# Kernel tuning notes

Hardware: AMD Instinct MI355X
Metric: run time of the kernel (lower is better)

The kernel has to match this reference:

```python
import jax, jax.numpy as jnp
import numpy as np

NUM_QUERIES = 256  # num_queries init arg
D = 256            # decoder_dim


def fps(xyz, n):
    """Furthest point sampling, matching the CUDA furthest_point_sample kernel:
    start at index 0, keep running min squared distance, pick argmax each step.
    xyz: [B, N, 3] -> indices [B, n] int32."""
    B, N, _ = xyz.shape

    def step(carry, _):
        dist, far = carry
        centroid = jnp.take_along_axis(xyz, far[:, None, None], axis=1)  # [B,1,3]
        d = jnp.sum((xyz - centroid) ** 2, axis=-1)                      # [B,N]
        dist = jnp.minimum(dist, d)
        return (dist, jnp.argmax(dist, axis=-1).astype(jnp.int32)), far

    init = (jnp.full((B, N), 1e10, xyz.dtype), jnp.zeros((B,), jnp.int32))
    _, inds = jax.lax.scan(step, init, None, length=n)
    return jnp.transpose(inds)  # [B, n]


def setup_inputs() -> dict:
    key = jax.random.key(0)
    ks = jax.random.split(key, 6)
    B, N = 64, 32768
    # scene coords in roughly [-3, 3]^3 meters
    encoder_xyz = jax.random.uniform(ks[0], (B, N, 3), jnp.float32) * 6.0 - 3.0
    pc_min = jnp.min(encoder_xyz, axis=1)  # [B,3]
    pc_max = jnp.max(encoder_xyz, axis=1)  # [B,3]
    gauss_B = jax.random.normal(ks[1], (3, D // 2), jnp.float32)  # fourier freqs
    W1 = jax.random.normal(ks[2], (D, D), jnp.float32) / np.sqrt(D)
    b1 = jnp.zeros((D,), jnp.float32)
    W2 = jax.random.normal(ks[3], (D, D), jnp.float32) / np.sqrt(D)
    b2 = jnp.zeros((D,), jnp.float32)
    return dict(encoder_xyz=encoder_xyz, pc_min=pc_min, pc_max=pc_max,
                gauss_B=gauss_B, W1=W1, b1=b1, W2=W2, b2=b2)


def reference(encoder_xyz, pc_min, pc_max, gauss_B, W1, b1, W2, b2):
    # --- query selection: FPS + gather (indices are non-differentiable) ---
    inds = fps(jax.lax.stop_gradient(encoder_xyz), NUM_QUERIES)          # [B,nq]
    query_xyz = jnp.take_along_axis(encoder_xyz, inds[..., None], axis=1)  # [B,nq,3]
    # --- PositionEmbeddingCoordsSine (fourier, normalize=True) ---
    norm = (query_xyz - pc_min[:, None, :]) / (pc_max - pc_min)[:, None, :]
    proj = (2.0 * jnp.pi) * jnp.einsum('bnd,df->bnf', norm, gauss_B)     # [B,nq,D/2]
    pos = jnp.concatenate([jnp.sin(proj), jnp.cos(proj)], axis=-1)       # [B,nq,D]
    pos = jnp.transpose(pos, (0, 2, 1))                                   # [B,D,nq]
    # --- query_projection GenericMLP: conv1x1 + ReLU, conv1x1 + output ReLU ---
    h = jax.nn.relu(jnp.einsum('bcn,dc->bdn', pos, W1) + b1[:, None])
    query_embed = jax.nn.relu(jnp.einsum('bcn,dc->bdn', h, W2) + b2[:, None])
    return query_xyz, query_embed
```

## Files before the change

kernel.cpp:

```cpp
#include <hip/hip_runtime.h>

#define FPS_N 32768
#define FPS_T 256
#define NBLK 8
#define PPB (FPS_N / NBLK)
#define PPT (PPB / FPS_T)
#define NCH (PPT / 4)
#define NQ 256
#define DD 256
#define NT 64
#define B_BATCH 64

#define WS_CLEAR_BYTES (B_BATCH * NQ * NBLK * 8)

__global__ __attribute__((amdgpu_flat_work_group_size(FPS_T, FPS_T),
                          amdgpu_waves_per_eu(2, 2)))
void fps_kernel(const float* __restrict__ xyz, float* __restrict__ qout,
                unsigned long long* __restrict__ gslot) {
  const int gid = blockIdx.x;
  const int xcd = gid & 7;
  const int s = gid >> 3;
  const int b = xcd + 8 * (s >> 3);
  const int q = s & 7;
  const int t = threadIdx.x;

  const float* __restrict__ base = xyz + (size_t)b * (FPS_N * 3);
  const float4* __restrict__ base4 =
      (const float4*)(base + (size_t)q * PPB * 3) + (size_t)t * (PPT * 3 / 4);
  float* qb = qout + (size_t)b * (NQ * 3);
  unsigned long long* bslot = gslot + (size_t)b * (NQ * NBLK);

  __shared__ unsigned long long sred[FPS_T / 64];
  __shared__ float4 bc;

  float4 C[PPT * 3 / 4];
#pragma unroll
  for (int i = 0; i < PPT * 3 / 4; ++i) C[i] = base4[i];
#pragma unroll
  for (int i = 0; i < PPT * 3 / 4; ++i) {
    asm volatile("" : "+v"(C[i].x), "+v"(C[i].y), "+v"(C[i].z), "+v"(C[i].w));
  }
  float4 Dst[NCH];
#pragma unroll
  for (int c = 0; c < NCH; ++c) Dst[c] = make_float4(1e10f, 1e10f, 1e10f, 1e10f);

  if (q == 0 && t == 0) { qb[0] = base[0]; qb[1] = base[1]; qb[2] = base[2]; }
  float cx = base[0], cy = base[1], cz = base[2];

#pragma unroll 1
  for (int j = 1; j < NQ; ++j) {
    float best = -1.0f;
    int bik = 0;

#pragma unroll
    for (int c = 0; c < NCH; ++c) {
      const float4 a4 = C[3 * c + 0];
      const float4 b4 = C[3 * c + 1];
      const float4 c4 = C[3 * c + 2];
      const float px[4] = {a4.x, a4.w, b4.z, c4.y};
      const float py[4] = {a4.y, b4.x, b4.w, c4.z};
      const float pz[4] = {a4.z, b4.y, c4.x, c4.w};
      const float dold[4] = {Dst[c].x, Dst[c].y, Dst[c].z, Dst[c].w};
      float dnew[4];
#pragma unroll
      for (int i = 0; i < 4; ++i) {
        const float dx = __fsub_rn(px[i], cx);
        const float dy = __fsub_rn(py[i], cy);
        const float dz = __fsub_rn(pz[i], cz);
        const float d = __fadd_rn(__fadd_rn(__fmul_rn(dx, dx), __fmul_rn(dy, dy)),
                                  __fmul_rn(dz, dz));
        const float nd = fminf(dold[i], d);
        dnew[i] = nd;
        if (nd > best) { best = nd; bik = c * 4 + i; }
      }
      Dst[c] = make_float4(dnew[0], dnew[1], dnew[2], dnew[3]);
    }
    int bi = q * PPB + t * PPT + bik;

#pragma unroll
    for (int off = 32; off; off >>= 1) {
      const float ov = __shfl_xor(best, off);
      const int oi = __shfl_xor(bi, off);
      if (ov > best || (ov == best && oi < bi)) { best = ov; bi = oi; }
    }
    if ((t & 63) == 0) {
      sred[t >> 6] = ((unsigned long long)(unsigned int)__float_as_int(best) << 32) |
                     (unsigned int)~(unsigned int)bi;
    }
    __syncthreads();

    if (t < 64) {
      unsigned long long p = sred[t & 3];
#pragma unroll
      for (int off = 1; off < 4; off <<= 1) {
        const unsigned long long o = __shfl_xor(p, off);
        if (o > p) p = o;
      }
      if (t == 0) {
        __hip_atomic_store(&bslot[j * NBLK + q], p, __ATOMIC_RELAXED,
                           __HIP_MEMORY_SCOPE_AGENT);
      }
      unsigned long long rp = 0;
      if (t < NBLK) {
        const unsigned long long* sl = &bslot[j * NBLK + t];
        do {
          rp = __hip_atomic_load(sl, __ATOMIC_RELAXED, __HIP_MEMORY_SCOPE_AGENT);
        } while (rp == 0ull);
      }
#pragma unroll
      for (int off = 1; off < NBLK; off <<= 1) {
        const unsigned long long o = __shfl_xor(rp, off);
        if (o > rp) rp = o;
      }
      if (t == 0) {
        const int gi = (int)~(unsigned int)(rp & 0xffffffffull);
        const float* cp = base + 3 * (size_t)gi;
        const float ncx = cp[0], ncy = cp[1], ncz = cp[2];
        bc = make_float4(ncx, ncy, ncz, 0.f);
        if (q == 0) { qb[3 * j + 0] = ncx; qb[3 * j + 1] = ncy; qb[3 * j + 2] = ncz; }
      }
    }
    __syncthreads();
    cx = bc.x; cy = bc.y; cz = bc.z;
  }
}

__global__ __launch_bounds__(256) void embed_mlp_kernel(
    const float* __restrict__ qxyz, const float* __restrict__ pcmin,
    const float* __restrict__ pcmax, const float* __restrict__ G,
    const float* __restrict__ W1, const float* __restrict__ b1,
    const float* __restrict__ W2, const float* __restrict__ b2,
    float* __restrict__ out) {
  const int b = blockIdx.x >> 2;
  const int n0 = (blockIdx.x & 3) * NT;
  const int tid = threadIdx.x;
  const int ty = tid >> 4, tx = tid & 15;

  __shared__ __align__(16) float P[DD][NT + 4];
  __shared__ __align__(16) float H[DD][NT + 4];
  __shared__ float snorm[NT][3];

  if (tid < NT) {
    const int n = n0 + tid;
    const float qx = qxyz[(size_t)b * (NQ * 3) + 3 * n + 0];
    const float qy = qxyz[(size_t)b * (NQ * 3) + 3 * n + 1];
    const float qz = qxyz[(size_t)b * (NQ * 3) + 3 * n + 2];
    snorm[tid][0] = (qx - pcmin[3 * b + 0]) / (pcmax[3 * b + 0] - pcmin[3 * b + 0]);
    snorm[tid][1] = (qy - pcmin[3 * b + 1]) / (pcmax[3 * b + 1] - pcmin[3 * b + 1]);
    snorm[tid][2] = (qz - pcmin[3 * b + 2]) / (pcmax[3 * b + 2] - pcmin[3 * b + 2]);
  }
  __syncthreads();

  {
    const int nn = tid & 63;
    const int fg = tid >> 6;
    const float nx = snorm[nn][0], ny = snorm[nn][1], nz = snorm[nn][2];
#pragma unroll 4
    for (int ff = 0; ff < 32; ++ff) {
      const int f = fg * 32 + ff;
      const float s = nx * G[f] + ny * G[128 + f] + nz * G[256 + f];
      const float proj = 6.28318530717958647692f * s;
      P[f][nn] = sinf(proj);
      P[f + 128][nn] = cosf(proj);
    }
  }
  __syncthreads();

  for (int layer = 0; layer < 2; ++layer) {
    const float* W = layer ? W2 : W1;
    const float* bias = layer ? b2 : b1;
    const float (*src)[NT + 4] = layer ? H : P;
    if (layer) __syncthreads();

    for (int dt = 0; dt < 4; ++dt) {
      float acc[4][4] = {};
      const float* wr0 = W + (size_t)(dt * 64 + ty * 4 + 0) * DD;
      const float* wr1 = wr0 + DD;
      const float* wr2 = wr1 + DD;
      const float* wr3 = wr2 + DD;
#pragma unroll 2
      for (int c = 0; c < DD; c += 4) {
        const float4 a0 = *(const float4*)(wr0 + c);
        const float4 a1 = *(const float4*)(wr1 + c);
        const float4 a2 = *(const float4*)(wr2 + c);
        const float4 a3 = *(const float4*)(wr3 + c);
        const float4 p0 = *(const float4*)&src[c + 0][tx * 4];
        const float4 p1 = *(const float4*)&src[c + 1][tx * 4];
        const float4 p2 = *(const float4*)&src[c + 2][tx * 4];
        const float4 p3 = *(const float4*)&src[c + 3][tx * 4];
        const float av[4][4] = {{a0.x, a0.y, a0.z, a0.w},
                                {a1.x, a1.y, a1.z, a1.w},
                                {a2.x, a2.y, a2.z, a2.w},
                                {a3.x, a3.y, a3.z, a3.w}};
        const float pv[4][4] = {{p0.x, p0.y, p0.z, p0.w},
                                {p1.x, p1.y, p1.z, p1.w},
                                {p2.x, p2.y, p2.z, p2.w},
                                {p3.x, p3.y, p3.z, p3.w}};
#pragma unroll
        for (int cj = 0; cj < 4; ++cj)
#pragma unroll
          for (int i = 0; i < 4; ++i)
#pragma unroll
            for (int k = 0; k < 4; ++k)
              acc[i][k] = fmaf(av[i][cj], pv[cj][k], acc[i][k]);
      }
      if (layer == 0) {
#pragma unroll
        for (int i = 0; i < 4; ++i) {
          const float bv = bias[dt * 64 + ty * 4 + i];
          float4 h;
          h.x = fmaxf(acc[i][0] + bv, 0.f);
          h.y = fmaxf(acc[i][1] + bv, 0.f);
          h.z = fmaxf(acc[i][2] + bv, 0.f);
          h.w = fmaxf(acc[i][3] + bv, 0.f);
          *(float4*)&H[dt * 64 + ty * 4 + i][tx * 4] = h;
        }
      } else {
        float* ob = out + (size_t)b * (DD * NQ);
#pragma unroll
        for (int i = 0; i < 4; ++i) {
          const float bv = bias[dt * 64 + ty * 4 + i];
          float4 h;
          h.x = fmaxf(acc[i][0] + bv, 0.f);
          h.y = fmaxf(acc[i][1] + bv, 0.f);
          h.z = fmaxf(acc[i][2] + bv, 0.f);
          h.w = fmaxf(acc[i][3] + bv, 0.f);
          *(float4*)(ob + (size_t)(dt * 64 + ty * 4 + i) * NQ + n0 + tx * 4) = h;
        }
      }
    }
  }
}

extern "C" void kernel_launch(void* const* d_in, const int* in_sizes, int n_in,
                              void* d_out, int out_size, void* d_ws, size_t ws_size,
                              hipStream_t stream) {
  (void)in_sizes; (void)n_in; (void)ws_size; (void)out_size;
  const float* xyz   = (const float*)d_in[0];
  const float* pcmin = (const float*)d_in[1];
  const float* pcmax = (const float*)d_in[2];
  const float* G     = (const float*)d_in[3];
  const float* W1    = (const float*)d_in[4];
  const float* b1    = (const float*)d_in[5];
  const float* W2    = (const float*)d_in[6];
  const float* b2    = (const float*)d_in[7];

  float* qxyz  = (float*)d_out;
  float* embed = qxyz + (size_t)B_BATCH * NQ * 3;

  unsigned long long* gslot = (unsigned long long*)d_ws;

  hipMemsetAsync(d_ws, 0, WS_CLEAR_BYTES, stream);

  hipLaunchKernelGGL(fps_kernel, dim3(B_BATCH * NBLK), dim3(FPS_T), 0, stream,
                     xyz, qxyz, gslot);
  hipLaunchKernelGGL(embed_mlp_kernel, dim3(B_BATCH * 4), dim3(256), 0, stream,
                     qxyz, pcmin, pcmax, G, W1, b1, W2, b2, embed);
}
```

Baseline: 569.5 us.

## Fuse FPS and embedding MLP into one kernel with chunked overlap via global slots

Merges the FPS and embedding/MLP kernels into a single launch. Extra blocks poll the per-iteration FPS reduction slots and process 16-query chunks as soon as they are finalised, recomputing selected indices from the slots. This overlaps the MLP with the serial FPS loop and removes the second launch. The cost is extra resident blocks and polling traffic, plus a deadlock risk if embed blocks are not co-resident with the FPS blocks. The embed blocks also inherit the FPS kernel's launch attributes (waves_per_eu 2).

```diff
diff --git a/kernel.cpp b/kernel.cpp
--- a/kernel.cpp
+++ b/kernel.cpp
@@ -8,226 +8,285 @@
 #define NCH (PPT / 4)
 #define NQ 256
 #define DD 256
-#define NT 64
 #define B_BATCH 64
+#define FPS_BLOCKS (B_BATCH * NBLK)
+#define EMB_BLOCKS (B_BATCH * 4)
+#define CHQ 16
+#define PLP 20
 
 #define WS_CLEAR_BYTES (B_BATCH * NQ * NBLK * 8)
 
 __global__ __attribute__((amdgpu_flat_work_group_size(FPS_T, FPS_T),
                           amdgpu_waves_per_eu(2, 2)))
-void fps_kernel(const float* __restrict__ xyz, float* __restrict__ qout,
-                unsigned long long* __restrict__ gslot) {
+void fps_embed_kernel(const float* __restrict__ xyz,
+                      const float* __restrict__ pcmin,
+                      const float* __restrict__ pcmax,
+                      const float* __restrict__ G,
+                      const float* __restrict__ W1, const float* __restrict__ b1,
+                      const float* __restrict__ W2, const float* __restrict__ b2,
+                      float* __restrict__ qout, float* __restrict__ eout,
+                      unsigned long long* __restrict__ gslot) {
   const int gid = blockIdx.x;
-  const int xcd = gid & 7;
-  const int s = gid >> 3;
-  const int b = xcd + 8 * (s >> 3);
-  const int q = s & 7;
   const int t = threadIdx.x;
-
-  const float* __restrict__ base = xyz + (size_t)b * (FPS_N * 3);
-  const float4* __restrict__ base4 =
-      (const float4*)(base + (size_t)q * PPB * 3) + (size_t)t * (PPT * 3 / 4);
-  float* qb = qout + (size_t)b * (NQ * 3);
-  unsigned long long* bslot = gslot + (size_t)b * (NQ * NBLK);
 
   __shared__ unsigned long long sred[FPS_T / 64];
   __shared__ float4 bc;
-
-  float4 C[PPT * 3 / 4];
-#pragma unroll
-  for (int i = 0; i < PPT * 3 / 4; ++i) C[i] = base4[i];
-#pragma unroll
-  for (int i = 0; i < PPT * 3 / 4; ++i) {
-    asm volatile("" : "+v"(C[i].x), "+v"(C[i].y), "+v"(C[i].z), "+v"(C[i].w));
-  }
-  float4 Dst[NCH];
-#pragma unroll
-  for (int c = 0; c < NCH; ++c) Dst[c] = make_float4(1e10f, 1e10f, 1e10f, 1e10f);
-
-  if (q == 0 && t == 0) { qb[0] = base[0]; qb[1] = base[1]; qb[2] = base[2]; }
-  float cx = base[0], cy = base[1], cz = base[2];
+  __shared__ __align__(16) float Pl[DD][PLP];
+  __shared__ __align__(16) float Hl[DD][PLP];
+  __shared__ int swidx[CHQ];
+  __shared__ float snrm[CHQ][3];
+
+  if (gid < FPS_BLOCKS) {
+    const int xcd = gid & 7;
+    const int s = gid >> 3;
+    const int b = xcd + 8 * (s >> 3);
+    const int q = s & 7;
+
+    const float* __restrict__ base = xyz + (size_t)b * (FPS_N * 3);
+    const float4* __restrict__ base4 =
+        (const float4*)(base + (size_t)q * PPB * 3) + (size_t)t * (PPT * 3 / 4);
+    float* qb = qout + (size_t)b * (NQ * 3);
+    unsigned long long* bslot = gslot + (size_t)b * (NQ * NBLK);
+
+    float4 C[PPT * 3 / 4];
+#pragma unroll
+    for (int i = 0; i < PPT * 3 / 4; ++i) C[i] = base4[i];
+#pragma unroll
+    for (int i = 0; i < PPT * 3 / 4; ++i) {
+      asm volatile("" : "+v"(C[i].x), "+v"(C[i].y), "+v"(C[i].z), "+v"(C[i].w));
+    }
+    float4 Dst[NCH];
+#pragma unroll
+    for (int c = 0; c < NCH; ++c) Dst[c] = make_float4(1e10f, 1e10f, 1e10f, 1e10f);
+
+    if (q == 0 && t == 0) { qb[0] = base[0]; qb[1] = base[1]; qb[2] = base[2]; }
+    float cx = base[0], cy = base[1], cz = base[2];
 
 #pragma unroll 1
-  for (int j = 1; j < NQ; ++j) {
-    float best = -1.0f;
-    int bik = 0;
-
-#pragma unroll
-    for (int c = 0; c < NCH; ++c) {
-      const float4 a4 = C[3 * c + 0];
-      const float4 b4 = C[3 * c + 1];
-      const float4 c4 = C[3 * c + 2];
-      const float px[4] = {a4.x, a4.w, b4.z, c4.y};
-      const float py[4] = {a4.y, b4.x, b4.w, c4.z};
-      const float pz[4] = {a4.z, b4.y, c4.x, c4.w};
-      const float dold[4] = {Dst[c].x, Dst[c].y, Dst[c].z, Dst[c].w};
-      float dnew[4];
-#pragma unroll
-      for (int i = 0; i < 4; ++i) {
-        const float dx = __fsub_rn(px[i], cx);
-        const float dy = __fsub_rn(py[i], cy);
-        const float dz = __fsub_rn(pz[i], cz);
-        const float d = __fadd_rn(__fadd_rn(__fmul_rn(dx, dx), __fmul_rn(dy, dy)),
-                                  __fmul_rn(dz, dz));
-        const float nd = fminf(dold[i], d);
-        dnew[i] = nd;
-        if (nd > best) { best = nd; bik = c * 4 + i; }
-      }
-      Dst[c] = make_float4(dnew[0], dnew[1], dnew[2], dnew[3]);
+    for (int j = 1; j < NQ; ++j) {
+      float best = -1.0f;
+      int bik = 0;
+
+#pragma unroll
+      for (int c = 0; c < NCH; ++c) {
+        const float4 a4 = C[3 * c + 0];
+        const float4 b4 = C[3 * c + 1];
+        const float4 c4 = C[3 * c + 2];
+        const float px[4] = {a4.x, a4.w, b4.z, c4.y};
+        const float py[4] = {a4.y, b4.x, b4.w, c4.z};
+        const float pz[4] = {a4.z, b4.y, c4.x, c4.w};
+        const float dold[4] = {Dst[c].x, Dst[c].y, Dst[c].z, Dst[c].w};
+        float dnew[4];
+#pragma unroll
+        for (int i = 0; i < 4; ++i) {
+          const float dx = __fsub_rn(px[i], cx);
+          const float dy = __fsub_rn(py[i], cy);
+          const float dz = __fsub_rn(pz[i], cz);
+          const float d = __fadd_rn(__fadd_rn(__fmul_rn(dx, dx), __fmul_rn(dy, dy)),
+                                    __fmul_rn(dz, dz));
+          const float nd = fminf(dold[i], d);
+          dnew[i] = nd;
+          if (nd > best) { best = nd; bik = c * 4 + i; }
+        }
+        Dst[c] = make_float4(dnew[0], dnew[1], dnew[2], dnew[3]);
+      }
+      int bi = q * PPB + t * PPT + bik;
+
+#pragma unroll
+      for (int off = 32; off; off >>= 1) {
+        const float ov = __shfl_xor(best, off);
+        const int oi = __shfl_xor(bi, off);
+        if (ov > best || (ov == best && oi < bi)) { best = ov; bi = oi; }
+      }
+      if ((t & 63) == 0) {
+        sred[t >> 6] = ((unsigned long long)(unsigned int)__float_as_int(best) << 32) |
+                       (unsigned int)~(unsigned int)bi;
+      }
+      __syncthreads();
+
+      if (t < 64) {
+        unsigned long long p = sred[t & 3];
+#pragma unroll
+        for (int off = 1; off < 4; off <<= 1) {
+          const unsigned long long o = __shfl_xor(p, off);
+          if (o > p) p = o;
+        }
+        if (t == 0) {
+          __hip_atomic_store(&bslot[j * NBLK + q], p, __ATOMIC_RELAXED,
+                             __HIP_MEMORY_SCOPE_AGENT);
+        }
+        unsigned long long rp = 0;
+        if (t < NBLK) {
+          const unsigned long long* sl = &bslot[j * NBLK + t];
+          do {
+            rp = __hip_atomic_load(sl, __ATOMIC_RELAXED, __HIP_MEMORY_SCOPE_AGENT);
+          } while (rp == 0ull);
+        }
+#pragma unroll
+        for (int off = 1; off < NBLK; off <<= 1) {
+          const unsigned long long o = __shfl_xor(rp, off);
+          if (o > rp) rp = o;
+        }
+        if (t == 0) {
+          const int gi = (int)~(unsigned int)(rp & 0xffffffffull);
+          const float* cp = base + 3 * (size_t)gi;
+          const float ncx = cp[0], ncy = cp[1], ncz = cp[2];
+          bc = make_float4(ncx, ncy, ncz, 0.f);
+          if (q == 0) { qb[3 * j + 0] = ncx; qb[3 * j + 1] = ncy; qb[3 * j + 2] = ncz; }
+        }
+      }
+      __syncthreads();
+      cx = bc.x; cy = bc.y; cz = bc.z;
     }
-    int bi = q * PPB + t * PPT + bik;
-
-#pragma unroll
-    for (int off = 32; off; off >>= 1) {
-      const float ov = __shfl_xor(best, off);
-      const int oi = __shfl_xor(bi, off);
-      if (ov > best || (ov == best && oi < bi)) { best = ov; bi = oi; }
-    }
-    if ((t & 63) == 0) {
-      sred[t >> 6] = ((unsigned long long)(unsigned int)__float_as_int(best) << 32) |
-                     (unsigned int)~(unsigned int)bi;
-    }
-    __syncthreads();
-
-    if (t < 64) {
-      unsigned long long p = sred[t & 3];
-#pragma unroll
-      for (int off = 1; off < 4; off <<= 1) {
+  } else {
+    const int eid = gid - FPS_BLOCKS;
+    const int b = eid >> 2;
+    const int n0 = (eid & 3) * 64;
+    const float* __restrict__ base = xyz + (size_t)b * (FPS_N * 3);
+    unsigned long long* bslot = gslot + (size_t)b * (NQ * NBLK);
+    float* ob = eout + (size_t)b * (DD * NQ);
+
+    const float mn0 = pcmin[3 * b + 0], mn1 = pcmin[3 * b + 1], mn2 = pcmin[3 * b + 2];
+    const float mx0 = pcmax[3 * b + 0], mx1 = pcmax[3 * b + 1], mx2 = pcmax[3 * b + 2];
+    const int ty = t >> 2, tx = t & 3;
+
+#pragma unroll 1
+    for (int ch = 0; ch < 64 / CHQ; ++ch) {
+      const int j0 = n0 + ch * CHQ;
+      if (t < NBLK) {
+        const unsigned long long* sl = &bslot[(size_t)(j0 + CHQ - 1) * NBLK + t];
+        while (__hip_atomic_load(sl, __ATOMIC_RELAXED,
+                                 __HIP_MEMORY_SCOPE_AGENT) == 0ull) {
+          __builtin_amdgcn_s_sleep(2);
+        }
+      }
+      __syncthreads();
+      unsigned long long p = 0xffffffffull;
+      if (t < 128) {
+        const int line = j0 + (t >> 3);
+        if (line > 0) {
+          p = __hip_atomic_load(&bslot[(size_t)line * NBLK + (t & 7)],
+                                __ATOMIC_RELAXED, __HIP_MEMORY_SCOPE_AGENT);
+        }
+      }
+#pragma unroll
+      for (int off = 1; off < 8; off <<= 1) {
         const unsigned long long o = __shfl_xor(p, off);
         if (o > p) p = o;
       }
-      if (t == 0) {
-        __hip_atomic_store(&bslot[j * NBLK + q], p, __ATOMIC_RELAXED,
-                           __HIP_MEMORY_SCOPE_AGENT);
-      }
-      unsigned long long rp = 0;
-      if (t < NBLK) {
-        const unsigned long long* sl = &bslot[j * NBLK + t];
-        do {
-          rp = __hip_atomic_load(sl, __ATOMIC_RELAXED, __HIP_MEMORY_SCOPE_AGENT);
-        } while (rp == 0ull);
-      }
-#pragma unroll
-      for (int off = 1; off < NBLK; off <<= 1) {
-        const unsigned long long o = __shfl_xor(rp, off);
-        if (o > rp) rp = o;
-      }
-      if (t == 0) {
-        const int gi = (int)~(unsigned int)(rp & 0xffffffffull);
-        const float* cp = base + 3 * (size_t)gi;
-        const float ncx = cp[0], ncy = cp[1], ncz = cp[2];
-        bc = make_float4(ncx, ncy, ncz, 0.f);
-        if (q == 0) { qb[3 * j + 0] = ncx; qb[3 * j + 1] = ncy; qb[3 * j + 2] = ncz; }
-      }
-    }
-    __syncthreads();
-    cx = bc.x; cy = bc.y; cz = bc.z;
-  }
-}
-
-__global__ __launch_bounds__(256) void embed_mlp_kernel(
-    const float* __restrict__ qxyz, const float* __restrict__ pcmin,
-    const float* __restrict__ pcmax, const float* __restrict__ G,
-    const float* __restrict__ W1, const float* __restrict__ b1,
-    const float* __restrict__ W2, const float* __restrict__ b2,
-    float* __restrict__ out) {
-  const int b = blockIdx.x >> 2;
-  const int n0 = (blockIdx.x & 3) * NT;
-  const int tid = threadIdx.x;
-  const int ty = tid >> 4, tx = tid & 15;
-
-  __shared__ __align__(16) float P[DD][NT + 4];
-  __shared__ __align__(16) float H[DD][NT + 4];
-  __shared__ float snorm[NT][3];
-
-  if (tid < NT) {
-    const int n = n0 + tid;
-    const float qx = qxyz[(size_t)b * (NQ * 3) + 3 * n + 0];
-    const float qy = qxyz[(size_t)b * (NQ * 3) + 3 * n + 1];
-    const float qz = qxyz[(size_t)b * (NQ * 3) + 3 * n + 2];
-    snorm[tid][0] = (qx - pcmin[3 * b + 0]) / (pcmax[3 * b + 0] - pcmin[3 * b + 0]);
-    snorm[tid][1] = (qy - pcmin[3 * b + 1]) / (pcmax[3 * b + 1] - pcmin[3 * b + 1]);
-    snorm[tid][2] = (qz - pcmin[3 * b + 2]) / (pcmax[3 * b + 2] - pcmin[3 * b + 2]);
-  }
-  __syncthreads();
-
-  {
-    const int nn = tid & 63;
-    const int fg = tid >> 6;
-    const float nx = snorm[nn][0], ny = snorm[nn][1], nz = snorm[nn][2];
-#pragma unroll 4
-    for (int ff = 0; ff < 32; ++ff) {
-      const int f = fg * 32 + ff;
-      const float s = nx * G[f] + ny * G[128 + f] + nz * G[256 + f];
-      const float proj = 6.28318530717958647692f * s;
-      P[f][nn] = sinf(proj);
-      P[f + 128][nn] = cosf(proj);
-    }
-  }
-  __syncthreads();
-
-  for (int layer = 0; layer < 2; ++layer) {
-    const float* W = layer ? W2 : W1;
-    const float* bias = layer ? b2 : b1;
-    const float (*src)[NT + 4] = layer ? H : P;
-    if (layer) __syncthreads();
-
-    for (int dt = 0; dt < 4; ++dt) {
-      float acc[4][4] = {};
-      const float* wr0 = W + (size_t)(dt * 64 + ty * 4 + 0) * DD;
-      const float* wr1 = wr0 + DD;
-      const float* wr2 = wr1 + DD;
-      const float* wr3 = wr2 + DD;
+      if (t < 128 && (t & 7) == 0) {
+        swidx[t >> 3] = (int)~(unsigned int)(p & 0xffffffffull);
+      }
+      __syncthreads();
+      if (t < CHQ) {
+        const int gi = swidx[t];
+        snrm[t][0] = (base[3 * gi + 0] - mn0) / (mx0 - mn0);
+        snrm[t][1] = (base[3 * gi + 1] - mn1) / (mx1 - mn1);
+        snrm[t][2] = (base[3 * gi + 2] - mn2) / (mx2 - mn2);
+      }
+      __syncthreads();
+      {
+        const int qi = t & 15;
+        const int fb = t >> 4;
+        const float nx = snrm[qi][0], ny = snrm[qi][1], nz = snrm[qi][2];
+#pragma unroll
+        for (int it = 0; it < 8; ++it) {
+          const int f = fb + it * 16;
+          const float sfv = nx * G[f] + ny * G[128 + f] + nz * G[256 + f];
+          const float pr = 6.28318530717958647692f * sfv;
+          Pl[f][qi] = sinf(pr);
+          Pl[f + 128][qi] = cosf(pr);
+        }
+      }
+      __syncthreads();
+      {
+        float acc[4][4] = {};
+        const float* wr0 = W1 + (size_t)(ty * 4 + 0) * DD;
+        const float* wr1 = wr0 + DD;
+        const float* wr2 = wr1 + DD;
+        const float* wr3 = wr2 + DD;
 #pragma unroll 2
-      for (int c = 0; c < DD; c += 4) {
-        const float4 a0 = *(const float4*)(wr0 + c);
-        const float4 a1 = *(const float4*)(wr1 + c);
-        const float4 a2 = *(const float4*)(wr2 + c);
-        const float4 a3 = *(const float4*)(wr3 + c);
-        const float4 p0 = *(const float4*)&src[c + 0][tx * 4];
-        const float4 p1 = *(const float4*)&src[c + 1][tx * 4];
-        const float4 p2 = *(const float4*)&src[c + 2][tx * 4];
-        const float4 p3 = *(const float4*)&src[c + 3][tx * 4];
-        const float av[4][4] = {{a0.x, a0.y, a0.z, a0.w},
-                                {a1.x, a1.y, a1.z, a1.w},
-                                {a2.x, a2.y, a2.z, a2.w},
-                                {a3.x, a3.y, a3.z, a3.w}};
-        const float pv[4][4] = {{p0.x, p0.y, p0.z, p0.w},
-                                {p1.x, p1.y, p1.z, p1.w},
-                                {p2.x, p2.y, p2.z, p2.w},
-                                {p3.x, p3.y, p3.z, p3.w}};
-#pragma unroll
-        for (int cj = 0; cj < 4; ++cj)
-#pragma unroll
-          for (int i = 0; i < 4; ++i)
-#pragma unroll
-            for (int k = 0; k < 4; ++k)
-              acc[i][k] = fmaf(av[i][cj], pv[cj][k], acc[i][k]);
-      }
-      if (layer == 0) {
+        for (int c = 0; c < DD; c += 4) {
+          const float4 a0 = *(const float4*)(wr0 + c);
+          const float4 a1 = *(const float4*)(wr1 + c);
+          const float4 a2 = *(const float4*)(wr2 + c);
+          const float4 a3 = *(const float4*)(wr3 + c);
+          const float4 p0 = *(const float4*)&Pl[c + 0][tx * 4];
+          const float4 p1 = *(const float4*)&Pl[c + 1][tx * 4];
+          const float4 p2 = *(const float4*)&Pl[c + 2][tx * 4];
+          const float4 p3 = *(const float4*)&Pl[c + 3][tx * 4];
+          const float av[4][4] = {{a0.x, a0.y, a0.z, a0.w},
+                                  {a1.x, a1.y, a1.z, a1.w},
+                                  {a2.x, a2.y, a2.z, a2.w},
+                                  {a3.x, a3.y, a3.z, a3.w}};
+          const float pv[4][4] = {{p0.x, p0.y, p0.z, p0.w},
+                                  {p1.x, p1.y, p1.z, p1.w},
+                                  {p2.x, p2.y, p2.z, p2.w},
+                                  {p3.x, p3.y, p3.z, p3.w}};
+#pragma unroll
+          for (int cj = 0; cj < 4; ++cj)
+#pragma unroll
+            for (int i = 0; i < 4; ++i)
+#pragma unroll
+              for (int k = 0; k < 4; ++k)
+                acc[i][k] = fmaf(av[i][cj], pv[cj][k], acc[i][k]);
+        }
 #pragma unroll
         for (int i = 0; i < 4; ++i) {
-          const float bv = bias[dt * 64 + ty * 4 + i];
+          const float bv = b1[ty * 4 + i];
           float4 h;
           h.x = fmaxf(acc[i][0] + bv, 0.f);
           h.y = fmaxf(acc[i][1] + bv, 0.f);
           h.z = fmaxf(acc[i][2] + bv, 0.f);
           h.w = fmaxf(acc[i][3] + bv, 0.f);
-          *(float4*)&H[dt * 64 + ty * 4 + i][tx * 4] = h;
-        }
-      } else {
-        float* ob = out + (size_t)b * (DD * NQ);
+          *(float4*)&Hl[ty * 4 + i][tx * 4] = h;
+        }
+      }
+      __syncthreads();
+      {
+        float acc[4][4] = {};
+        const float* wr0 = W2 + (size_t)(ty * 4 + 0) * DD;
+        const float* wr1 = wr0 + DD;
+        const float* wr2 = wr1 + DD;
+        const float* wr3 = wr2 + DD;
+#pragma unroll 2
+        for (int c = 0; c < DD; c += 4) {
+          const float4 a0 = *(const float4*)(wr0 + c);
+          const float4 a1 = *(const float4*)(wr1 + c);
+          const float4 a2 = *(const float4*)(wr2 + c);
+          const float4 a3 = *(const float4*)(wr3 + c);
+          const float4 p0 = *(const float4*)&Hl[c + 0][tx * 4];
+          const float4 p1 = *(const float4*)&Hl[c + 1][tx * 4];
+          const float4 p2 = *(const float4*)&Hl[c + 2][tx * 4];
+          const float4 p3 = *(const float4*)&Hl[c + 3][tx * 4];
+          const float av[4][4] = {{a0.x, a0.y, a0.z, a0.w},
+                                  {a1.x, a1.y, a1.z, a1.w},
+                                  {a2.x, a2.y, a2.z, a2.w},
+                                  {a3.x, a3.y, a3.z, a3.w}};
+          const float pv[4][4] = {{p0.x, p0.y, p0.z, p0.w},
+                                  {p1.x, p1.y, p1.z, p1.w},
+                                  {p2.x, p2.y, p2.z, p2.w},
+                                  {p3.x, p3.y, p3.z, p3.w}};
+#pragma unroll
+          for (int cj = 0; cj < 4; ++cj)
+#pragma unroll
+            for (int i = 0; i < 4; ++i)
+#pragma unroll
+              for (int k = 0; k < 4; ++k)
+                acc[i][k] = fmaf(av[i][cj], pv[cj][k], acc[i][k]);
+        }
 #pragma unroll
         for (int i = 0; i < 4; ++i) {
-          const float bv = bias[dt * 64 + ty * 4 + i];
+          const float bv = b2[ty * 4 + i];
           float4 h;
           h.x = fmaxf(acc[i][0] + bv, 0.f);
           h.y = fmaxf(acc[i][1] + bv, 0.f);
           h.z = fmaxf(acc[i][2] + bv, 0.f);
           h.w = fmaxf(acc[i][3] + bv, 0.f);
-          *(float4*)(ob + (size_t)(dt * 64 + ty * 4 + i) * NQ + n0 + tx * 4) = h;
-        }
-      }
+          *(float4*)(ob + (size_t)(ty * 4 + i) * NQ + j0 + tx * 4) = h;
+        }
+      }
+      __syncthreads();
     }
   }
 }
@@ -252,8 +311,7 @@
 
   hipMemsetAsync(d_ws, 0, WS_CLEAR_BYTES, stream);
 
-  hipLaunchKernelGGL(fps_kernel, dim3(B_BATCH * NBLK), dim3(FPS_T), 0, stream,
-                     xyz, qxyz, gslot);
-  hipLaunchKernelGGL(embed_mlp_kernel, dim3(B_BATCH * 4), dim3(256), 0, stream,
-                     qxyz, pcmin, pcmax, G, W1, b1, W2, b2, embed);
+  hipLaunchKernelGGL(fps_embed_kernel, dim3(FPS_BLOCKS + EMB_BLOCKS),
+                     dim3(FPS_T), 0, stream, xyz, pcmin, pcmax, G,
+                     W1, b1, W2, b2, qxyz, embed, gslot);
 }
```

Measured after the change: 622.4 us. +9.3%, slower.
